# Performance work log

Measured on AMD Instinct MI355X. Metric: run time of the kernel, lower is better.

The kernel has to match this reference:

```python
import jax, jax.numpy as jnp
import numpy as np

N_NODES = 100000
N_EDGES = 1600000
D_NODE = 32
D_EDGE = 16
D_OUT = 32
L2_EPS = 1e-12  # tf.math.l2_normalize default epsilon


def setup_inputs() -> dict:
    key = jax.random.key(0)
    k_h, k_e, k_w, k_s, k_d = jax.random.split(key, 5)
    h = jax.random.normal(k_h, (N_NODES, D_NODE), dtype=jnp.float32)
    e = jax.random.normal(k_e, (N_EDGES, D_EDGE), dtype=jnp.float32)
    # Dense(output_dim) kernel over concat(node, edge) features
    W = jax.random.normal(k_w, (D_NODE + D_EDGE, D_OUT), dtype=jnp.float32) * 0.1
    b = jnp.zeros((D_OUT,), dtype=jnp.float32)
    src = jax.random.randint(k_s, (N_EDGES,), 0, N_NODES, dtype=jnp.int32)
    dst = jax.random.randint(k_d, (N_EDGES,), 0, N_NODES, dtype=jnp.int32)
    return {"h": h, "e": e, "W": W, "b": b, "src": src, "dst": dst}


def reference(h, e, W, b, src, dst):
    # message: m = concat(h[src], e)              [E, D+De]
    # reduce:  new_h = mean over (self_msg, mailbox) of Dense(msg)
    # Dense is affine (activation=None), so Dense(mean) == mean(Dense): one GEMM.
    n = h.shape[0]
    msg = jnp.concatenate([h[src], e], axis=-1)                      # [E, D+De]
    agg = jax.ops.segment_sum(msg, dst, num_segments=n)              # [N, D+De]
    deg = jax.ops.segment_sum(jnp.ones_like(dst, dtype=h.dtype), dst, num_segments=n)
    self_msg = jnp.concatenate([h, jnp.zeros((n, e.shape[1]), h.dtype)], axis=-1)
    mean_msg = (self_msg + agg) / (deg[:, None] + 1.0)               # self counts in the mean
    new_h = mean_msg @ W + b                                         # [N, D_OUT]
    # activation=None -> identity; then tf.math.l2_normalize(axis=-1)
    sq = jnp.sum(new_h * new_h, axis=-1, keepdims=True)
    return new_h * jax.lax.rsqrt(jnp.maximum(sq, L2_EPS))
```

## Files before the change

### kernel.cpp

```cpp
#include <hip/hip_runtime.h>

#define D_NODE 32
#define D_EDGE 16
#define D_IN   48
#define D_OUT  32
#define L2_EPS 1e-12f

#define NPB       128
#define BKT_SHIFT 7
#define MAX_NB    4096
#define CH        8192
#define CTH       1024
#define EPT       (CH / CTH)
#define GR        128
#define TILE      512
#define ATH       512
#define PST       513


__global__ __launch_bounds__(CTH) void k_chunkhist(
    const int* __restrict__ dst, int* __restrict__ counts2d, int n_edges, int nb)
{
    extern __shared__ int c[];
    for (int i = threadIdx.x; i < nb; i += CTH) c[i] = 0;
    __syncthreads();
    int base = blockIdx.x * CH + threadIdx.x;
    #pragma unroll
    for (int k = 0; k < EPT; ++k) {
        int i = base + k * CTH;
        if (i < n_edges) atomicAdd(&c[dst[i] >> BKT_SHIFT], 1);
    }
    __syncthreads();
    int* row = counts2d + (size_t)blockIdx.x * nb;
    for (int i = threadIdx.x; i < nb; i += CTH) row[i] = c[i];
}

__global__ __launch_bounds__(256) void k_partial(
    const int* __restrict__ counts2d, int* __restrict__ partial, int nb, int nc)
{
    int b = blockIdx.x * 256 + threadIdx.x;
    if (b >= nb) return;
    int g = blockIdx.y;
    int c0 = g * GR, c1 = min(c0 + GR, nc);
    int s = 0;
    #pragma unroll 4
    for (int c = c0; c < c1; ++c) s += counts2d[(size_t)c * nb + b];
    partial[(size_t)g * nb + b] = s;
}

__global__ __launch_bounds__(1024) void k_offsets(
    int* __restrict__ partial, int* __restrict__ offsets, int nb, int ng)
{
    __shared__ int s[1024];
    const int PT = MAX_NB / 1024;
    int t = threadIdx.x;
    int tot[PT];
    int ts = 0;
    #pragma unroll
    for (int j = 0; j < PT; ++j) {
        int b = t * PT + j;
        int v = 0;
        if (b < nb) for (int g = 0; g < ng; ++g) v += partial[(size_t)g * nb + b];
        tot[j] = v; ts += v;
    }
    s[t] = ts;
    __syncthreads();
    for (int off = 1; off < 1024; off <<= 1) {
        int u = (t >= off) ? s[t - off] : 0;
        __syncthreads();
        s[t] += u;
        __syncthreads();
    }
    if (t == 1023) offsets[nb] = s[1023];
    int run = s[t] - ts;
    #pragma unroll
    for (int j = 0; j < PT; ++j) {
        int b = t * PT + j;
        if (b < nb) {
            offsets[b] = run;
            int r2 = run;
            for (int g = 0; g < ng; ++g) {
                int v = partial[(size_t)g * nb + b];
                partial[(size_t)g * nb + b] = r2;
                r2 += v;
            }
            run += tot[j];
        }
    }
}

__global__ __launch_bounds__(256) void k_base2d(
    int* __restrict__ counts2d, const int* __restrict__ partial, int nb, int nc)
{
    int b = blockIdx.x * 256 + threadIdx.x;
    if (b >= nb) return;
    int g = blockIdx.y;
    int run = partial[(size_t)g * nb + b];
    int c0 = g * GR, c1 = min(c0 + GR, nc);
    #pragma unroll 4
    for (int c = c0; c < c1; ++c) {
        size_t idx = (size_t)c * nb + b;
        int v = counts2d[idx];
        counts2d[idx] = run;
        run += v;
    }
}

__global__ __launch_bounds__(CTH) void k_scatter(
    const int* __restrict__ dst, const int* __restrict__ src,
    const int* __restrict__ base2d, int2* __restrict__ meta2, int n_edges, int nb)
{
    extern __shared__ int sm[];
    int* lbase = sm;
    int* lrank = sm + nb;
    const int* brow = base2d + (size_t)blockIdx.x * nb;
    for (int i = threadIdx.x; i < nb; i += CTH) { lbase[i] = brow[i]; lrank[i] = 0; }
    __syncthreads();
    int base = blockIdx.x * CH + threadIdx.x;
    #pragma unroll
    for (int k = 0; k < EPT; ++k) {
        int i = base + k * CTH;
        if (i < n_edges) {
            int d = dst[i];
            int bkt = d >> BKT_SHIFT;
            int r = atomicAdd(&lrank[bkt], 1);
            int slot = lbase[bkt] + r;
            meta2[slot] = make_int2(src[i] | ((d & (NPB - 1)) << 20), i);
        }
    }
}

__global__ __launch_bounds__(ATH) void k_accum(
    const float* __restrict__ h, const float4* __restrict__ e4,
    const float* __restrict__ W, const float* __restrict__ b,
    const int* __restrict__ offsets, const int2* __restrict__ meta2,
    float* __restrict__ out, int n_nodes)
{
    __shared__ float Ws[D_IN * D_OUT];
    __shared__ float bs[D_OUT];
    __shared__ int meta_s[TILE];
    __shared__ int2 csr[TILE];
    __shared__ int cnt[NPB], cnt2[NPB], offs[NPB];
    __shared__ float pool[16 * PST];

    for (int i = threadIdx.x; i < D_IN * D_OUT; i += ATH) Ws[i] = W[i];
    if (threadIdx.x < D_OUT) bs[threadIdx.x] = b[threadIdx.x];
    __syncthreads();

    int g  = threadIdx.x >> 2;
    int jg = threadIdx.x & 3;

    float4 ha0 = make_float4(0.f, 0.f, 0.f, 0.f);
    float4 ha1 = make_float4(0.f, 0.f, 0.f, 0.f);
    float4 ea  = make_float4(0.f, 0.f, 0.f, 0.f);
    float deg = 0.f;

    int b0 = offsets[blockIdx.x], b1 = offsets[blockIdx.x + 1];
    for (int t0 = b0; t0 < b1; t0 += TILE) {
        int tn = min(TILE, b1 - t0);
        if (threadIdx.x < NPB) { cnt[threadIdx.x] = 0; cnt2[threadIdx.x] = 0; }
        __syncthreads();
        if (threadIdx.x < tn) {
            int2 m2 = meta2[t0 + threadIdx.x];
            meta_s[threadIdx.x] = m2.x;
            const float4* er = e4 + (size_t)m2.y * 4;
            float4 v0 = er[0], v1 = er[1], v2 = er[2], v3 = er[3];
            int sb = threadIdx.x;
            pool[ 0 * PST + sb] = v0.x; pool[ 1 * PST + sb] = v0.y;
            pool[ 2 * PST + sb] = v0.z; pool[ 3 * PST + sb] = v0.w;
            pool[ 4 * PST + sb] = v1.x; pool[ 5 * PST + sb] = v1.y;
            pool[ 6 * PST + sb] = v1.z; pool[ 7 * PST + sb] = v1.w;
            pool[ 8 * PST + sb] = v2.x; pool[ 9 * PST + sb] = v2.y;
            pool[10 * PST + sb] = v2.z; pool[11 * PST + sb] = v2.w;
            pool[12 * PST + sb] = v3.x; pool[13 * PST + sb] = v3.y;
            pool[14 * PST + sb] = v3.z; pool[15 * PST + sb] = v3.w;
        }
        __syncthreads();
        if (threadIdx.x < tn)
            atomicAdd(&cnt[(meta_s[threadIdx.x] >> 20) & (NPB - 1)], 1);
        __syncthreads();
        if (threadIdx.x < 64) {
            int c0 = cnt[2 * threadIdx.x];
            int c1 = cnt[2 * threadIdx.x + 1];
            int p = c0 + c1;
            int x = p;
            #pragma unroll
            for (int o = 1; o < 64; o <<= 1) {
                int y = __shfl_up(x, o);
                if (threadIdx.x >= o) x += y;
            }
            int basex = x - p;
            offs[2 * threadIdx.x]     = basex;
            offs[2 * threadIdx.x + 1] = basex + c0;
        }
        __syncthreads();
        if (threadIdx.x < tn) {
            int mv = meta_s[threadIdx.x];
            int dl = (mv >> 20) & (NPB - 1);
            int r = atomicAdd(&cnt2[dl], 1);
            csr[offs[dl] + r] = make_int2(mv, threadIdx.x);
        }
        __syncthreads();
        int myc = cnt[g];
        int mybase = offs[g];
        deg += (float)myc;
        #pragma unroll 4
        for (int s = 0; s < myc; ++s) {
            int2 c = csr[mybase + s];
            const float4* hr = reinterpret_cast<const float4*>(
                h + (size_t)(c.x & 0xFFFFF) * D_NODE) + 2 * jg;
            float4 h0 = hr[0], h1 = hr[1];
            int sb = c.y;
            float e0 = pool[(4 * jg + 0) * PST + sb];
            float e1 = pool[(4 * jg + 1) * PST + sb];
            float e2 = pool[(4 * jg + 2) * PST + sb];
            float e3 = pool[(4 * jg + 3) * PST + sb];
            ha0.x += h0.x; ha0.y += h0.y; ha0.z += h0.z; ha0.w += h0.w;
            ha1.x += h1.x; ha1.y += h1.y; ha1.z += h1.z; ha1.w += h1.w;
            ea.x += e0; ea.y += e1; ea.z += e2; ea.w += e3;
        }
        __syncthreads();
    }

    float (*mrow)[D_IN + 1] = reinterpret_cast<float (*)[D_IN + 1]>(pool);
    __syncthreads();

    int node = blockIdx.x * NPB + g;
    if (node < n_nodes) {
        float inv = 1.f / (deg + 1.f);
        const float4* hs = reinterpret_cast<const float4*>(
            h + (size_t)node * D_NODE) + 2 * jg;
        float4 s0 = hs[0], s1 = hs[1];
        mrow[g][8 * jg + 0] = (ha0.x + s0.x) * inv;
        mrow[g][8 * jg + 1] = (ha0.y + s0.y) * inv;
        mrow[g][8 * jg + 2] = (ha0.z + s0.z) * inv;
        mrow[g][8 * jg + 3] = (ha0.w + s0.w) * inv;
        mrow[g][8 * jg + 4] = (ha1.x + s1.x) * inv;
        mrow[g][8 * jg + 5] = (ha1.y + s1.y) * inv;
        mrow[g][8 * jg + 6] = (ha1.z + s1.z) * inv;
        mrow[g][8 * jg + 7] = (ha1.w + s1.w) * inv;
        mrow[g][D_NODE + 4 * jg + 0] = ea.x * inv;
        mrow[g][D_NODE + 4 * jg + 1] = ea.y * inv;
        mrow[g][D_NODE + 4 * jg + 2] = ea.z * inv;
        mrow[g][D_NODE + 4 * jg + 3] = ea.w * inv;
    }
    __syncthreads();
    if (node >= n_nodes) return;

    const float* row = mrow[g];
    float a[8];
    #pragma unroll
    for (int q = 0; q < 8; ++q) a[q] = bs[jg * 8 + q];
    #pragma unroll
    for (int k = 0; k < D_IN; ++k) {
        float mk = row[k];
        const float* w = Ws + k * D_OUT + jg * 8;
        #pragma unroll
        for (int q = 0; q < 8; ++q) a[q] += mk * w[q];
    }
    float sq = 0.f;
    #pragma unroll
    for (int q = 0; q < 8; ++q) sq += a[q] * a[q];
    sq += __shfl_xor(sq, 1);
    sq += __shfl_xor(sq, 2);
    float r = rsqrtf(fmaxf(sq, L2_EPS));
    float4* o4 = reinterpret_cast<float4*>(out + (size_t)node * D_OUT) + 2 * jg;
    o4[0] = make_float4(a[0] * r, a[1] * r, a[2] * r, a[3] * r);
    o4[1] = make_float4(a[4] * r, a[5] * r, a[6] * r, a[7] * r);
}

__global__ __launch_bounds__(256) void scatter_kernel(
    const float* __restrict__ h, const float* __restrict__ e,
    const int* __restrict__ src, const int* __restrict__ dst,
    float* __restrict__ agg, float* __restrict__ deg, int n_edges)
{
    int tid  = blockIdx.x * blockDim.x + threadIdx.x;
    int edge = tid >> 4;
    int c    = tid & 15;
    if (edge >= n_edges) return;
    int s = src[edge], d = dst[edge];
    float v0 = h[(size_t)s * D_NODE + c];
    float v1 = h[(size_t)s * D_NODE + 16 + c];
    float v2 = e[(size_t)edge * D_EDGE + c];
    float* row = agg + (size_t)d * D_IN;
    atomicAdd(row + c, v0);
    atomicAdd(row + 16 + c, v1);
    atomicAdd(row + 32 + c, v2);
    if (c == 0) atomicAdd(deg + d, 1.0f);
}

__global__ __launch_bounds__(256) void node_kernel(
    const float* __restrict__ h, const float* __restrict__ W, const float* __restrict__ b,
    const float* __restrict__ agg, const float* __restrict__ deg,
    float* __restrict__ out, int n_nodes)
{
    __shared__ float Ws[D_IN * D_OUT];
    __shared__ float bs[D_OUT];
    for (int i = threadIdx.x; i < D_IN * D_OUT; i += blockDim.x) Ws[i] = W[i];
    if (threadIdx.x < D_OUT) bs[threadIdx.x] = b[threadIdx.x];
    __syncthreads();
    int node = blockIdx.x * blockDim.x + threadIdx.x;
    if (node >= n_nodes) return;
    const float4* h4 = reinterpret_cast<const float4*>(h + (size_t)node * D_NODE);
    const float4* a4 = reinterpret_cast<const float4*>(agg + (size_t)node * D_IN);
    float inv = 1.0f / (deg[node] + 1.0f);
    float m[D_IN];
    #pragma unroll
    for (int k = 0; k < D_NODE / 4; ++k) {
        float4 hv = h4[k]; float4 av = a4[k];
        m[4*k+0] = (hv.x + av.x) * inv; m[4*k+1] = (hv.y + av.y) * inv;
        m[4*k+2] = (hv.z + av.z) * inv; m[4*k+3] = (hv.w + av.w) * inv;
    }
    #pragma unroll
    for (int k = D_NODE / 4; k < D_IN / 4; ++k) {
        float4 av = a4[k];
        m[4*k+0] = av.x * inv; m[4*k+1] = av.y * inv;
        m[4*k+2] = av.z * inv; m[4*k+3] = av.w * inv;
    }
    float acc[D_OUT];
    #pragma unroll
    for (int j = 0; j < D_OUT; ++j) acc[j] = bs[j];
    #pragma unroll
    for (int k = 0; k < D_IN; ++k) {
        float mk = m[k];
        #pragma unroll
        for (int j = 0; j < D_OUT; ++j) acc[j] += mk * Ws[k * D_OUT + j];
    }
    float sq = 0.0f;
    #pragma unroll
    for (int j = 0; j < D_OUT; ++j) sq += acc[j] * acc[j];
    float r = rsqrtf(fmaxf(sq, L2_EPS));
    float4* o4 = reinterpret_cast<float4*>(out + (size_t)node * D_OUT);
    #pragma unroll
    for (int j = 0; j < D_OUT / 4; ++j) {
        float4 v;
        v.x = acc[4*j+0] * r; v.y = acc[4*j+1] * r;
        v.z = acc[4*j+2] * r; v.w = acc[4*j+3] * r;
        o4[j] = v;
    }
}

extern "C" void kernel_launch(void* const* d_in, const int* in_sizes, int n_in,
                              void* d_out, int out_size, void* d_ws, size_t ws_size,
                              hipStream_t stream) {
    const float* h   = (const float*)d_in[0];
    const float* e   = (const float*)d_in[1];
    const float* W   = (const float*)d_in[2];
    const float* b   = (const float*)d_in[3];
    const int*   src = (const int*)d_in[4];
    const int*   dst = (const int*)d_in[5];
    float* out = (float*)d_out;

    const int n_nodes = in_sizes[0] / D_NODE;
    const int n_edges = in_sizes[4];

    const int nb  = (n_nodes + NPB - 1) / NPB;
    const int nc  = (n_edges + CH - 1) / CH;
    const int ng  = (nc + GR - 1) / GR;
    const int nbt = (nb + 255) / 256;

    size_t o_counts2d = 0;
    size_t o_partial  = o_counts2d + (size_t)nc * nb;
    size_t o_offsets  = o_partial + (size_t)ng * nb;
    size_t o_meta2    = (o_offsets + (size_t)nb + 1 + 1) & ~(size_t)1;
    size_t need       = (o_meta2 + (size_t)n_edges * 2) * sizeof(int);

    if (nb <= MAX_NB && n_nodes < (1 << 20) && need <= ws_size && n_edges > 0) {
        int* ws_i     = (int*)d_ws;
        int* counts2d = ws_i + o_counts2d;
        int* partial  = ws_i + o_partial;
        int* offsets  = ws_i + o_offsets;
        int2* meta2   = (int2*)(ws_i + o_meta2);

        dim3 g2(nbt, ng);
        k_chunkhist<<<nc, CTH, (size_t)nb * sizeof(int), stream>>>(
            dst, counts2d, n_edges, nb);
        k_partial<<<g2, 256, 0, stream>>>(counts2d, partial, nb, nc);
        k_offsets<<<1, 1024, 0, stream>>>(partial, offsets, nb, ng);
        k_base2d<<<g2, 256, 0, stream>>>(counts2d, partial, nb, nc);
        k_scatter<<<nc, CTH, (size_t)2 * nb * sizeof(int), stream>>>(
            dst, src, counts2d, meta2, n_edges, nb);
        k_accum<<<nb, ATH, 0, stream>>>(
            h, (const float4*)e, W, b, offsets, meta2, out, n_nodes);
    } else {
        float* agg = (float*)d_ws;
        float* deg = agg + (size_t)n_nodes * D_IN;
        hipMemsetAsync(d_ws, 0, (size_t)n_nodes * (D_IN + 1) * sizeof(float), stream);
        long long threads = (long long)n_edges * 16;
        scatter_kernel<<<(int)((threads + 255) / 256), 256, 0, stream>>>(h, e, src, dst, agg, deg, n_edges);
        node_kernel<<<(n_nodes + 255) / 256, 256, 0, stream>>>(h, W, b, agg, deg, out, n_nodes);
    }
}
```

Measured before the change: 122.5 us.

## Prefetch next tile's edge metadata and features into registers, use float4 LDS pool

Software-pipelines the accumulate kernel: the next tile's meta entries and edge-feature rows are loaded into registers while the current tile is bucketed and summed. The per-tile sync count drops because the meta_s staging buffer is removed, counters are reset inside existing phases, and the cnt histogram is built in the same phase as the pool store. The edge-feature pool becomes a padded float4 layout so each thread reads its four edge values with one vector LDS access instead of four scalar reads. The cost is more live registers, which may lower occupancy, and more intricate reset ordering.

```diff
diff --git a/kernel.cpp b/kernel.cpp
--- a/kernel.cpp
+++ b/kernel.cpp
@@ -15,7 +15,6 @@
 #define GR        128
 #define TILE      512
 #define ATH       512
-#define PST       513
 
 
 __global__ __launch_bounds__(CTH) void k_chunkhist(
@@ -138,13 +137,26 @@
 {
     __shared__ float Ws[D_IN * D_OUT];
     __shared__ float bs[D_OUT];
-    __shared__ int meta_s[TILE];
     __shared__ int2 csr[TILE];
     __shared__ int cnt[NPB], cnt2[NPB], offs[NPB];
-    __shared__ float pool[16 * PST];
+    __shared__ float4 pool4[4 * (TILE + 1)];
+
+    int b0 = offsets[blockIdx.x], b1 = offsets[blockIdx.x + 1];
+
+    int2 m2 = make_int2(0, 0);
+    float4 v0 = make_float4(0.f, 0.f, 0.f, 0.f), v1 = v0, v2 = v0, v3 = v0;
+    {
+        int tn0 = min(TILE, b1 - b0);
+        if ((int)threadIdx.x < tn0) {
+            m2 = meta2[b0 + threadIdx.x];
+            const float4* er = e4 + (size_t)m2.y * 4;
+            v0 = er[0]; v1 = er[1]; v2 = er[2]; v3 = er[3];
+        }
+    }
 
     for (int i = threadIdx.x; i < D_IN * D_OUT; i += ATH) Ws[i] = W[i];
     if (threadIdx.x < D_OUT) bs[threadIdx.x] = b[threadIdx.x];
+    if (threadIdx.x < NPB) { cnt[threadIdx.x] = 0; cnt2[threadIdx.x] = 0; }
     __syncthreads();
 
     int g  = threadIdx.x >> 2;
@@ -155,30 +167,24 @@
     float4 ea  = make_float4(0.f, 0.f, 0.f, 0.f);
     float deg = 0.f;
 
-    int b0 = offsets[blockIdx.x], b1 = offsets[blockIdx.x + 1];
     for (int t0 = b0; t0 < b1; t0 += TILE) {
-        int tn = min(TILE, b1 - t0);
-        if (threadIdx.x < NPB) { cnt[threadIdx.x] = 0; cnt2[threadIdx.x] = 0; }
-        __syncthreads();
-        if (threadIdx.x < tn) {
-            int2 m2 = meta2[t0 + threadIdx.x];
-            meta_s[threadIdx.x] = m2.x;
-            const float4* er = e4 + (size_t)m2.y * 4;
-            float4 v0 = er[0], v1 = er[1], v2 = er[2], v3 = er[3];
-            int sb = threadIdx.x;
-            pool[ 0 * PST + sb] = v0.x; pool[ 1 * PST + sb] = v0.y;
-            pool[ 2 * PST + sb] = v0.z; pool[ 3 * PST + sb] = v0.w;
-            pool[ 4 * PST + sb] = v1.x; pool[ 5 * PST + sb] = v1.y;
-            pool[ 6 * PST + sb] = v1.z; pool[ 7 * PST + sb] = v1.w;
-            pool[ 8 * PST + sb] = v2.x; pool[ 9 * PST + sb] = v2.y;
-            pool[10 * PST + sb] = v2.z; pool[11 * PST + sb] = v2.w;
-            pool[12 * PST + sb] = v3.x; pool[13 * PST + sb] = v3.y;
-            pool[14 * PST + sb] = v3.z; pool[15 * PST + sb] = v3.w;
-        }
-        __syncthreads();
-        if (threadIdx.x < tn)
-            atomicAdd(&cnt[(meta_s[threadIdx.x] >> 20) & (NPB - 1)], 1);
-        __syncthreads();
+        int tn  = min(TILE, b1 - t0);
+        int t1  = t0 + TILE;
+        int ntn = (t1 < b1) ? min(TILE, b1 - t1) : 0;
+        int mv  = m2.x;
+        int dl  = (mv >> 20) & (NPB - 1);
+
+        if ((int)threadIdx.x < ntn) m2 = meta2[t1 + threadIdx.x];
+        if ((int)threadIdx.x < tn) {
+            float4* pr = pool4 + threadIdx.x;
+            pr[0]              = v0;
+            pr[TILE + 1]       = v1;
+            pr[2 * (TILE + 1)] = v2;
+            pr[3 * (TILE + 1)] = v3;
+            atomicAdd(&cnt[dl], 1);
+        }
+        __syncthreads();
+
         if (threadIdx.x < 64) {
             int c0 = cnt[2 * threadIdx.x];
             int c1 = cnt[2 * threadIdx.x + 1];
@@ -192,37 +198,41 @@
             int basex = x - p;
             offs[2 * threadIdx.x]     = basex;
             offs[2 * threadIdx.x + 1] = basex + c0;
-        }
-        __syncthreads();
-        if (threadIdx.x < tn) {
-            int mv = meta_s[threadIdx.x];
-            int dl = (mv >> 20) & (NPB - 1);
+        } else if (threadIdx.x < 64 + NPB) {
+            cnt2[threadIdx.x - 64] = 0;
+        }
+        int myc = cnt[g];
+        __syncthreads();
+
+        int mybase = offs[g];
+        if ((int)threadIdx.x < tn) {
             int r = atomicAdd(&cnt2[dl], 1);
             csr[offs[dl] + r] = make_int2(mv, threadIdx.x);
         }
-        __syncthreads();
-        int myc = cnt[g];
-        int mybase = offs[g];
+        if ((int)threadIdx.x < ntn) {
+            const float4* er = e4 + (size_t)m2.y * 4;
+            v0 = er[0]; v1 = er[1]; v2 = er[2]; v3 = er[3];
+        }
+        if (threadIdx.x < NPB) cnt[threadIdx.x] = 0;
         deg += (float)myc;
+        __syncthreads();
+
+        const float4* poolj = pool4 + jg * (TILE + 1);
         #pragma unroll 4
         for (int s = 0; s < myc; ++s) {
             int2 c = csr[mybase + s];
             const float4* hr = reinterpret_cast<const float4*>(
                 h + (size_t)(c.x & 0xFFFFF) * D_NODE) + 2 * jg;
             float4 h0 = hr[0], h1 = hr[1];
-            int sb = c.y;
-            float e0 = pool[(4 * jg + 0) * PST + sb];
-            float e1 = pool[(4 * jg + 1) * PST + sb];
-            float e2 = pool[(4 * jg + 2) * PST + sb];
-            float e3 = pool[(4 * jg + 3) * PST + sb];
+            float4 ev = poolj[c.y];
             ha0.x += h0.x; ha0.y += h0.y; ha0.z += h0.z; ha0.w += h0.w;
             ha1.x += h1.x; ha1.y += h1.y; ha1.z += h1.z; ha1.w += h1.w;
-            ea.x += e0; ea.y += e1; ea.z += e2; ea.w += e3;
-        }
-        __syncthreads();
-    }
-
-    float (*mrow)[D_IN + 1] = reinterpret_cast<float (*)[D_IN + 1]>(pool);
+            ea.x  += ev.x; ea.y  += ev.y; ea.z  += ev.z; ea.w  += ev.w;
+        }
+        __syncthreads();
+    }
+
+    float (*mrow)[D_IN + 1] = reinterpret_cast<float (*)[D_IN + 1]>(pool4);
     __syncthreads();
 
     int node = blockIdx.x * NPB + g;
```

Result: no change. 122.9 us (+0.3%).
